# Optimization experiments

Measured on AMD Instinct MI355X. Metric: run time of the kernel, lower is better.

Reference implementation:

```python
import jax, jax.numpy as jnp
import numpy as np

B, N, T, F_IN = 4, 2000, 24, 16
H = 128          # hidden_dim
E = 64000        # num edges
C = 6            # num_classes (LOS A-F)
NH = 1           # num_horizons


def setup_inputs() -> dict:
    key = jax.random.key(0)
    ks = jax.random.split(key, 16)
    s = lambda *sh: 1.0 / np.sqrt(sh[-1])
    inp = {
        "node_features": jax.random.normal(ks[0], (B, N, T, F_IN), dtype=jnp.float32),
        "edge_index": jax.random.randint(ks[1], (2, E), 0, N, dtype=jnp.int64),
        # GRU (single layer, unidirectional), PyTorch gate order r,z,n
        "W_ih": jax.random.normal(ks[2], (3 * H, F_IN), dtype=jnp.float32) * s(3 * H, F_IN),
        "W_hh": jax.random.normal(ks[3], (3 * H, H), dtype=jnp.float32) * s(3 * H, H),
        "b_ih": jnp.zeros((3 * H,), dtype=jnp.float32),
        "b_hh": jnp.zeros((3 * H,), dtype=jnp.float32),
        # two GCN layers (H -> H)
        "gcn_W1": jax.random.normal(ks[4], (H, H), dtype=jnp.float32) * s(H, H),
        "gcn_b1": jnp.zeros((H,), dtype=jnp.float32),
        "gcn_W2": jax.random.normal(ks[5], (H, H), dtype=jnp.float32) * s(H, H),
        "gcn_b2": jnp.zeros((H,), dtype=jnp.float32),
        # LayerNorms
        "ln_g1": jnp.ones((H,), dtype=jnp.float32),
        "ln_b1": jnp.zeros((H,), dtype=jnp.float32),
        "ln_g2": jnp.ones((H,), dtype=jnp.float32),
        "ln_b2": jnp.zeros((H,), dtype=jnp.float32),
        # classifier: Linear(2H -> H), ReLU, Linear(H -> C*NH)
        "cls_W1": jax.random.normal(ks[6], (H, 2 * H), dtype=jnp.float32) * s(H, 2 * H),
        "cls_b1": jnp.zeros((H,), dtype=jnp.float32),
        "cls_W2": jax.random.normal(ks[7], (C * NH, H), dtype=jnp.float32) * s(C * NH, H),
        "cls_b2": jnp.zeros((C * NH,), dtype=jnp.float32),
    }
    return inp


def _gru(x, W_ih, W_hh, b_ih, b_hh):
    # x: [BN, T, F] -> final hidden [BN, H]
    BN = x.shape[0]
    gi = jnp.einsum('btf,gf->btg', x, W_ih) + b_ih           # [BN, T, 3H]
    h0 = jnp.zeros((BN, H), dtype=x.dtype)

    def step(h, gi_t):
        gh = h @ W_hh.T + b_hh
        ir, iz, inn = jnp.split(gi_t, 3, axis=-1)
        hr, hz, hn = jnp.split(gh, 3, axis=-1)
        r = jax.nn.sigmoid(ir + hr)
        z = jax.nn.sigmoid(iz + hz)
        n = jnp.tanh(inn + r * hn)
        h_new = (1.0 - z) * n + z * h
        return h_new, None

    h_fin, _ = jax.lax.scan(step, h0, jnp.swapaxes(gi, 0, 1))  # scan over time
    return h_fin


def _gcn(x, src, dst, W, b):
    # x: [B, N, D]; normalized adjacency aggregation then linear
    deg = jax.ops.segment_sum(jnp.ones((src.shape[0],), x.dtype), dst, num_segments=N)
    deg = jnp.maximum(deg, 1.0)
    dis = deg ** -0.5
    norm = dis[src] * dis[dst]                                # [E]
    msg = x[:, src, :] * norm[None, :, None]                  # [B, E, D]
    agg = jax.vmap(lambda m: jax.ops.segment_sum(m, dst, num_segments=N))(msg)
    return agg @ W.T + b


def _layernorm(x, g, b, eps=1e-5):
    mu = jnp.mean(x, axis=-1, keepdims=True)
    var = jnp.var(x, axis=-1, keepdims=True)
    return (x - mu) * jax.lax.rsqrt(var + eps) * g + b


def reference(node_features, edge_index, W_ih, W_hh, b_ih, b_hh,
              gcn_W1, gcn_b1, gcn_W2, gcn_b2,
              ln_g1, ln_b1, ln_g2, ln_b2,
              cls_W1, cls_b1, cls_W2, cls_b2):
    src, dst = edge_index[0], edge_index[1]
    x = node_features.reshape(B * N, T, F_IN)
    temporal = _gru(x, W_ih, W_hh, b_ih, b_hh).reshape(B, N, H)   # [B, N, H]

    s = _gcn(temporal, src, dst, gcn_W1, gcn_b1)
    s = jax.nn.relu(_layernorm(s, ln_g1, ln_b1))
    s = _gcn(s, src, dst, gcn_W2, gcn_b2)
    s = jax.nn.relu(_layernorm(s, ln_g2, ln_b2))

    combined = jnp.concatenate([temporal, s], axis=-1)            # [B, N, 2H]
    h = jax.nn.relu(combined @ cls_W1.T + cls_b1)
    logits = h @ cls_W2.T + cls_b2
    return logits.reshape(B, N, NH, C)
```

## Files before the change

kernel.cpp:

```cpp
#include <hip/hip_runtime.h>
#include <math.h>

#define BB  4
#define NN  2000
#define TT  24
#define FIN 16
#define HH  128
#define EE  64000
#define CC  6
#define BN  (BB*NN)
#define SLOTC 128

typedef _Float16 f16x8 __attribute__((ext_vector_type(8)));
typedef float f32x4 __attribute__((ext_vector_type(4)));

#define HP2 136
#define GRUB 500

__global__ __launch_bounds__(512) void gru_fill_kernel(
    const float* __restrict__ x,
    const float* __restrict__ W_hh,
    const float* __restrict__ W_ih,
    const float* __restrict__ b_ih, const float* __restrict__ b_hh,
    const float* __restrict__ gW1,
    const float* __restrict__ cW1,
    _Float16* __restrict__ tw16,
    _Float16* __restrict__ tc16,
    const int* __restrict__ src, const int* __restrict__ dst,
    int* __restrict__ cnt, int* __restrict__ slots)
{
    const int tid  = threadIdx.x;

    if (blockIdx.x >= GRUB) {
        int e = (blockIdx.x - GRUB) * 512 + tid;
        if (e < EE) {
            int d = dst[e], s = src[e];
            int pos = atomicAdd(&cnt[d], 1);
            if (pos < SLOTC) slots[d * SLOTC + pos] = s;
        }
        return;
    }

    const int lane = tid & 63;
    const int w    = tid >> 6;
    const int l15  = lane & 15;
    const int lg   = lane >> 4;
    const int m0   = blockIdx.x * 16;
    const int u    = w * 16 + l15;

    __shared__ __align__(16) unsigned short Hhi[2][16][HP2];
    __shared__ __align__(16) unsigned short Xhi[TT][16][FIN];

    f16x8 Bh[3][4];
    #pragma unroll
    for (int g = 0; g < 3; ++g) {
        const int col = g * 128 + u;
        #pragma unroll
        for (int kf = 0; kf < 4; ++kf) {
            const float* wp = W_hh + col * 128 + kf * 32 + lg * 8;
            float4 c0 = *(const float4*)wp;
            float4 c1 = *(const float4*)(wp + 4);
            f16x8 b;
            b[0] = (_Float16)c0.x; b[1] = (_Float16)c0.y;
            b[2] = (_Float16)c0.z; b[3] = (_Float16)c0.w;
            b[4] = (_Float16)c1.x; b[5] = (_Float16)c1.y;
            b[6] = (_Float16)c1.z; b[7] = (_Float16)c1.w;
            Bh[g][kf] = b;
        }
    }
    f16x8 Bi[3];
    #pragma unroll
    for (int g = 0; g < 3; ++g) {
        const int col = g * 128 + u;
        f16x8 b;
        #pragma unroll
        for (int i = 0; i < 8; ++i) b[i] = (_Float16)0.0f;
        if (lg < 2) {
            const float* wp = W_ih + col * 16 + lg * 8;
            float4 c0 = *(const float4*)wp;
            float4 c1 = *(const float4*)(wp + 4);
            b[0] = (_Float16)c0.x; b[1] = (_Float16)c0.y;
            b[2] = (_Float16)c0.z; b[3] = (_Float16)c0.w;
            b[4] = (_Float16)c1.x; b[5] = (_Float16)c1.y;
            b[6] = (_Float16)c1.z; b[7] = (_Float16)c1.w;
        } else if (lg == 2) {
            float bias = b_ih[col] + ((g < 2) ? b_hh[col] : 0.0f);
            b[0] = (_Float16)bias;
        }
        Bi[g] = b;
    }

    const float bhn = b_hh[256 + u];
    float hprev[4] = {0.0f, 0.0f, 0.0f, 0.0f};

    for (int i = tid; i < TT * 16 * FIN; i += 512) {
        int t   = i >> 8;
        int rem = i & 255;
        int seq = rem >> 4;
        int f   = rem & 15;
        float v = x[(size_t)(m0 + seq) * (TT * FIN) + t * FIN + f];
        _Float16 hb = (_Float16)v;
        Xhi[t][seq][f] = *(unsigned short*)&hb;
    }
    for (int i = tid; i < 16 * HP2; i += 512) (&Hhi[0][0][0])[i] = 0;
    __syncthreads();

    const f32x4 Z4 = (f32x4){0.f, 0.f, 0.f, 0.f};
    f32x4 aR, aZ, aH, aI;

#define IH_SHADOW(tt) do { \
        f16x8 axh; \
        _Float16 zz = (_Float16)0.0f; \
        axh = (f16x8){zz,zz,zz,zz,zz,zz,zz,zz}; \
        if (lg < 2) { \
            axh = *(const f16x8*)&Xhi[tt][l15][lg * 8]; \
        } else if (lg == 2) { \
            axh[0] = (_Float16)1.0f; \
        } \
        aR = __builtin_amdgcn_mfma_f32_16x16x32_f16(axh, Bi[0], Z4, 0, 0, 0); \
        aZ = __builtin_amdgcn_mfma_f32_16x16x32_f16(axh, Bi[1], Z4, 0, 0, 0); \
        aI = __builtin_amdgcn_mfma_f32_16x16x32_f16(axh, Bi[2], Z4, 0, 0, 0); \
        aH = Z4; \
    } while (0)

    IH_SHADOW(0);

    for (int t = 0; t < TT; ++t) {
        const int rb = t & 1, wb = rb ^ 1;

        #pragma unroll
        for (int kf = 0; kf < 4; ++kf) {
            const int ko = kf * 32 + lg * 8;
            f16x8 ahh = *(const f16x8*)&Hhi[rb][l15][ko];
            aR = __builtin_amdgcn_mfma_f32_16x16x32_f16(ahh, Bh[0][kf], aR, 0, 0, 0);
            aZ = __builtin_amdgcn_mfma_f32_16x16x32_f16(ahh, Bh[1][kf], aZ, 0, 0, 0);
            aH = __builtin_amdgcn_mfma_f32_16x16x32_f16(ahh, Bh[2][kf], aH, 0, 0, 0);
        }

        f32x4 aRv = aR, aZv = aZ, aHv = aH, aIv = aI;

        #pragma unroll
        for (int p = 0; p < 4; ++p) {
            float r = __builtin_amdgcn_rcpf(1.0f + __expf(-aRv[p]));
            float z = __builtin_amdgcn_rcpf(1.0f + __expf(-aZv[p]));
            float pre = fmaf(r, aHv[p] + bhn, aIv[p]);
            float e2 = __expf(2.0f * pre);
            float n = fmaf(-2.0f, __builtin_amdgcn_rcpf(e2 + 1.0f), 1.0f);
            float h = fmaf(z, hprev[p] - n, n);
            hprev[p] = h;
            _Float16 hb = (_Float16)h;
            const int seq = lg * 4 + p;
            Hhi[wb][seq][u] = *(unsigned short*)&hb;
        }

        if (t + 1 < TT) IH_SHADOW(t + 1);
        __syncthreads();
    }
#undef IH_SHADOW

    {
        f32x4 accw = Z4, accc = Z4;
        #pragma unroll
        for (int kf = 0; kf < 4; ++kf) {
            const int ko = kf * 32 + lg * 8;
            f16x8 ah = *(const f16x8*)&Hhi[0][l15][ko];

            const float* wp = gW1 + (size_t)u * 128 + ko;
            float4 c0 = *(const float4*)wp;
            float4 c1 = *(const float4*)(wp + 4);
            f16x8 bw;
            bw[0] = (_Float16)c0.x; bw[1] = (_Float16)c0.y;
            bw[2] = (_Float16)c0.z; bw[3] = (_Float16)c0.w;
            bw[4] = (_Float16)c1.x; bw[5] = (_Float16)c1.y;
            bw[6] = (_Float16)c1.z; bw[7] = (_Float16)c1.w;
            accw = __builtin_amdgcn_mfma_f32_16x16x32_f16(ah, bw, accw, 0, 0, 0);

            const float* cp = cW1 + (size_t)u * 256 + ko;
            float4 d0 = *(const float4*)cp;
            float4 d1 = *(const float4*)(cp + 4);
            f16x8 bc;
            bc[0] = (_Float16)d0.x; bc[1] = (_Float16)d0.y;
            bc[2] = (_Float16)d0.z; bc[3] = (_Float16)d0.w;
            bc[4] = (_Float16)d1.x; bc[5] = (_Float16)d1.y;
            bc[6] = (_Float16)d1.z; bc[7] = (_Float16)d1.w;
            accc = __builtin_amdgcn_mfma_f32_16x16x32_f16(ah, bc, accc, 0, 0, 0);
        }
        #pragma unroll
        for (int p = 0; p < 4; ++p) {
            const int row = lg * 4 + p;
            tw16[(size_t)(m0 + row) * HH + u] = (_Float16)accw[p];
            tc16[(size_t)(m0 + row) * HH + u] = (_Float16)accc[p];
        }
    }
}

__global__ __launch_bounds__(1024) void gcn1b_kernel(
    const _Float16* __restrict__ tw,
    const int* __restrict__ cnt, const int* __restrict__ slots,
    const float* __restrict__ gb1,
    const float* __restrict__ lg1, const float* __restrict__ lb1,
    const float* __restrict__ gW2,
    _Float16* __restrict__ sw)
{
    const int tid  = threadIdx.x;
    const int nd   = tid >> 8;
    const int t8   = tid & 255;
    const int j    = t8 & 127;
    const int half = t8 >> 7;
    const int n0   = blockIdx.x * 4;
    const int n    = n0 + nd;

    __shared__ float disL[2048];
    for (int i = tid; i < 2048; i += 1024)
        disL[i] = rsqrtf(fmaxf((float)cnt[i], 1.0f));
    __syncthreads();

    const int deg = min(cnt[n], SLOTC);
    const float rd = disL[n];
    const int mid = (deg + 1) >> 1;
    int e        = half ? mid : 0;
    const int e1 = half ? deg : mid;
    const int* sl = slots + (size_t)n * SLOTC;

    float a0 = 0.f, a1 = 0.f, a2 = 0.f, a3 = 0.f;
    for (; e + 1 < e1; e += 2) {
        int   s0 = sl[e],      s1i = sl[e + 1];
        float m0 = disL[s0],   m1  = disL[s1i];
        const _Float16* p0 = tw + (size_t)s0  * HH + j;
        const _Float16* p1 = tw + (size_t)s1i * HH + j;
        a0 = fmaf(m0, (float)p0[0],       a0); a1 = fmaf(m0, (float)p0[NN*HH],   a1);
        a2 = fmaf(m0, (float)p0[2*NN*HH], a2); a3 = fmaf(m0, (float)p0[3*NN*HH], a3);
        a0 = fmaf(m1, (float)p1[0],       a0); a1 = fmaf(m1, (float)p1[NN*HH],   a1);
        a2 = fmaf(m1, (float)p1[2*NN*HH], a2); a3 = fmaf(m1, (float)p1[3*NN*HH], a3);
    }
    if (e < e1) {
        int s0 = sl[e]; float m0 = disL[s0];
        const _Float16* p0 = tw + (size_t)s0 * HH + j;
        a0 = fmaf(m0, (float)p0[0],       a0); a1 = fmaf(m0, (float)p0[NN*HH],   a1);
        a2 = fmaf(m0, (float)p0[2*NN*HH], a2); a3 = fmaf(m0, (float)p0[3*NN*HH], a3);
    }

    __shared__ __align__(16) float pagg[4][BB][HH];
    __shared__ __align__(16) float agg[4][BB][HH];
    if (half) {
        pagg[nd][0][j] = a0; pagg[nd][1][j] = a1;
        pagg[nd][2][j] = a2; pagg[nd][3][j] = a3;
    }
    __syncthreads();
    if (!half) {
        agg[nd][0][j] = a0 + pagg[nd][0][j]; agg[nd][1][j] = a1 + pagg[nd][1][j];
        agg[nd][2][j] = a2 + pagg[nd][2][j]; agg[nd][3][j] = a3 + pagg[nd][3][j];
    }
    __syncthreads();

    const float bj = gb1[j];
    const int b0 = half * 2, b1 = half * 2 + 1;
    float c0 = fmaf(rd, agg[nd][b0][j], bj);
    float c1 = fmaf(rd, agg[nd][b1][j], bj);

    const int lane = t8 & 63, wv = (t8 >> 6) & 1;
    __shared__ float red[4][2][2][2][2];
    {
        float s1 = c0, s2 = c0 * c0;
        for (int off = 32; off >= 1; off >>= 1) { s1 += __shfl_down(s1, off); s2 += __shfl_down(s2, off); }
        if (lane == 0) { red[nd][half][wv][0][0] = s1; red[nd][half][wv][0][1] = s2; }
        s1 = c1; s2 = c1 * c1;
        for (int off = 32; off >= 1; off >>= 1) { s1 += __shfl_down(s1, off); s2 += __shfl_down(s2, off); }
        if (lane == 0) { red[nd][half][wv][1][0] = s1; red[nd][half][wv][1][1] = s2; }
    }
    __syncthreads();

    __shared__ __align__(16) unsigned short sL[16][HP2];
    const float gj = lg1[j], btj = lb1[j];
    #pragma unroll
    for (int q = 0; q < 2; ++q) {
        float cv = q ? c1 : c0;
        float s1 = red[nd][half][0][q][0] + red[nd][half][1][q][0];
        float s2 = red[nd][half][0][q][1] + red[nd][half][1][q][1];
        float mu = s1 * (1.0f / HH);
        float var = s2 * (1.0f / HH) - mu * mu;
        float y = (cv - mu) * rsqrtf(var + 1e-5f) * gj + btj;
        _Float16 hv = (_Float16)fmaxf(y, 0.0f);
        sL[nd * 4 + (half * 2 + q)][j] = *(unsigned short*)&hv;
    }
    __syncthreads();

    if (tid < 512) {
        const int w = tid >> 6, l15 = tid & 15, lg = (tid & 63) >> 4;
        const int u = w * 16 + l15;
        f32x4 acc = (f32x4){0.f, 0.f, 0.f, 0.f};
        #pragma unroll
        for (int kf = 0; kf < 4; ++kf) {
            const int ko = kf * 32 + lg * 8;
            f16x8 a = *(const f16x8*)&sL[l15][ko];
            const float* wp = gW2 + (size_t)u * 128 + ko;
            float4 c0v = *(const float4*)wp;
            float4 c1v = *(const float4*)(wp + 4);
            f16x8 b;
            b[0] = (_Float16)c0v.x; b[1] = (_Float16)c0v.y;
            b[2] = (_Float16)c0v.z; b[3] = (_Float16)c0v.w;
            b[4] = (_Float16)c1v.x; b[5] = (_Float16)c1v.y;
            b[6] = (_Float16)c1v.z; b[7] = (_Float16)c1v.w;
            acc = __builtin_amdgcn_mfma_f32_16x16x32_f16(a, b, acc, 0, 0, 0);
        }
        #pragma unroll
        for (int p = 0; p < 4; ++p) {
            const int r = lg * 4 + p;
            const int nd2 = r >> 2, b2 = r & 3;
            sw[((size_t)b2 * NN + n0 + nd2) * HH + u] = (_Float16)acc[p];
        }
    }
}

__global__ __launch_bounds__(1024) void gcn2b_cls_kernel(
    const _Float16* __restrict__ sw,
    const int* __restrict__ cnt, const int* __restrict__ slots,
    const float* __restrict__ gb2,
    const float* __restrict__ lg2, const float* __restrict__ lb2,
    const float* __restrict__ cW1,
    const _Float16* __restrict__ tc,
    const float* __restrict__ cb1,
    const float* __restrict__ cW2,
    const float* __restrict__ cb2,
    float* __restrict__ out)
{
    const int tid  = threadIdx.x;
    const int nd   = tid >> 8;
    const int t8   = tid & 255;
    const int j    = t8 & 127;
    const int half = t8 >> 7;
    const int n0   = blockIdx.x * 4;
    const int n    = n0 + nd;

    __shared__ float disL[2048];
    for (int i = tid; i < 2048; i += 1024)
        disL[i] = rsqrtf(fmaxf((float)cnt[i], 1.0f));
    __syncthreads();

    const int deg = min(cnt[n], SLOTC);
    const float rd = disL[n];
    const int mid = (deg + 1) >> 1;
    int e        = half ? mid : 0;
    const int e1 = half ? deg : mid;
    const int* sl = slots + (size_t)n * SLOTC;

    float a0 = 0.f, a1 = 0.f, a2 = 0.f, a3 = 0.f;
    for (; e + 1 < e1; e += 2) {
        int   s0 = sl[e],      s1i = sl[e + 1];
        float m0 = disL[s0],   m1  = disL[s1i];
        const _Float16* p0 = sw + (size_t)s0  * HH + j;
        const _Float16* p1 = sw + (size_t)s1i * HH + j;
        a0 = fmaf(m0, (float)p0[0],       a0); a1 = fmaf(m0, (float)p0[NN*HH],   a1);
        a2 = fmaf(m0, (float)p0[2*NN*HH], a2); a3 = fmaf(m0, (float)p0[3*NN*HH], a3);
        a0 = fmaf(m1, (float)p1[0],       a0); a1 = fmaf(m1, (float)p1[NN*HH],   a1);
        a2 = fmaf(m1, (float)p1[2*NN*HH], a2); a3 = fmaf(m1, (float)p1[3*NN*HH], a3);
    }
    if (e < e1) {
        int s0 = sl[e]; float m0 = disL[s0];
        const _Float16* p0 = sw + (size_t)s0 * HH + j;
        a0 = fmaf(m0, (float)p0[0],       a0); a1 = fmaf(m0, (float)p0[NN*HH],   a1);
        a2 = fmaf(m0, (float)p0[2*NN*HH], a2); a3 = fmaf(m0, (float)p0[3*NN*HH], a3);
    }

    __shared__ __align__(16) float pagg[4][BB][HH];
    __shared__ __align__(16) float agg[4][BB][HH];
    if (half) {
        pagg[nd][0][j] = a0; pagg[nd][1][j] = a1;
        pagg[nd][2][j] = a2; pagg[nd][3][j] = a3;
    }
    __syncthreads();
    if (!half) {
        agg[nd][0][j] = a0 + pagg[nd][0][j]; agg[nd][1][j] = a1 + pagg[nd][1][j];
        agg[nd][2][j] = a2 + pagg[nd][2][j]; agg[nd][3][j] = a3 + pagg[nd][3][j];
    }
    __syncthreads();

    const float bj = gb2[j];
    const int b0 = half * 2, b1 = half * 2 + 1;
    float c0 = fmaf(rd, agg[nd][b0][j], bj);
    float c1 = fmaf(rd, agg[nd][b1][j], bj);

    const int lane = t8 & 63, wv = (t8 >> 6) & 1;
    __shared__ float red[4][2][2][2][2];
    {
        float s1 = c0, s2 = c0 * c0;
        for (int off = 32; off >= 1; off >>= 1) { s1 += __shfl_down(s1, off); s2 += __shfl_down(s2, off); }
        if (lane == 0) { red[nd][half][wv][0][0] = s1; red[nd][half][wv][0][1] = s2; }
        s1 = c1; s2 = c1 * c1;
        for (int off = 32; off >= 1; off >>= 1) { s1 += __shfl_down(s1, off); s2 += __shfl_down(s2, off); }
        if (lane == 0) { red[nd][half][wv][1][0] = s1; red[nd][half][wv][1][1] = s2; }
    }
    __syncthreads();

    __shared__ __align__(16) unsigned short s2L[16][HP2];
    const float gj = lg2[j], btj = lb2[j];
    #pragma unroll
    for (int q = 0; q < 2; ++q) {
        float cv = q ? c1 : c0;
        float s1 = red[nd][half][0][q][0] + red[nd][half][1][q][0];
        float s2 = red[nd][half][0][q][1] + red[nd][half][1][q][1];
        float mu = s1 * (1.0f / HH);
        float var = s2 * (1.0f / HH) - mu * mu;
        float y = (cv - mu) * rsqrtf(var + 1e-5f) * gj + btj;
        _Float16 hv = (_Float16)fmaxf(y, 0.0f);
        s2L[nd * 4 + (half * 2 + q)][j] = *(unsigned short*)&hv;
    }
    __syncthreads();

    __shared__ __align__(16) float h1L[16][132];
    if (tid < 512) {
        const int w = tid >> 6, l15 = tid & 15, lg = (tid & 63) >> 4;
        const int u = w * 16 + l15;
        f32x4 acc = (f32x4){0.f, 0.f, 0.f, 0.f};
        #pragma unroll
        for (int kf = 0; kf < 4; ++kf) {
            const int ko = kf * 32 + lg * 8;
            f16x8 a = *(const f16x8*)&s2L[l15][ko];
            const float* cp = cW1 + (size_t)u * 256 + 128 + ko;
            float4 d0 = *(const float4*)cp;
            float4 d1 = *(const float4*)(cp + 4);
            f16x8 b;
            b[0] = (_Float16)d0.x; b[1] = (_Float16)d0.y;
            b[2] = (_Float16)d0.z; b[3] = (_Float16)d0.w;
            b[4] = (_Float16)d1.x; b[5] = (_Float16)d1.y;
            b[6] = (_Float16)d1.z; b[7] = (_Float16)d1.w;
            acc = __builtin_amdgcn_mfma_f32_16x16x32_f16(a, b, acc, 0, 0, 0);
        }
        const float bu = cb1[u];
        #pragma unroll
        for (int p = 0; p < 4; ++p) {
            const int r = lg * 4 + p;
            const int nd2 = r >> 2, b2 = r & 3;
            const size_t flat = (size_t)b2 * NN + n0 + nd2;
            float tcv = (float)tc[flat * HH + u];
            h1L[r][u] = fmaxf(acc[p] + tcv + bu, 0.0f);
        }
    }
    __syncthreads();

    if (tid < 16 * CC) {
        int r = tid / CC, cc = tid - r * CC;
        const int nd2 = r >> 2, b2 = r & 3;
        const size_t flat = (size_t)b2 * NN + n0 + nd2;
        float a = cb2[cc];
        const float* wp = cW2 + cc * HH;
        #pragma unroll 4
        for (int k = 0; k < HH; ++k) a = fmaf(wp[k], h1L[r][k], a);
        out[flat * CC + cc] = a;
    }
}

extern "C" void kernel_launch(void* const* d_in, const int* in_sizes, int n_in,
                              void* d_out, int out_size, void* d_ws, size_t ws_size,
                              hipStream_t stream) {
    const float* x    = (const float*)d_in[0];
    const int*   ei   = (const int*)  d_in[1];
    const float* W_ih = (const float*)d_in[2];
    const float* W_hh = (const float*)d_in[3];
    const float* b_ih = (const float*)d_in[4];
    const float* b_hh = (const float*)d_in[5];
    const float* gW1  = (const float*)d_in[6];
    const float* gb1  = (const float*)d_in[7];
    const float* gW2  = (const float*)d_in[8];
    const float* gb2  = (const float*)d_in[9];
    const float* lg1  = (const float*)d_in[10];
    const float* lb1  = (const float*)d_in[11];
    const float* lg2  = (const float*)d_in[12];
    const float* lb2  = (const float*)d_in[13];
    const float* cW1  = (const float*)d_in[14];
    const float* cb1  = (const float*)d_in[15];
    const float* cW2  = (const float*)d_in[16];
    const float* cb2  = (const float*)d_in[17];
    float* out = (float*)d_out;

    float* ws = (float*)d_ws;
    _Float16* tw16 = (_Float16*)ws;  ws += (size_t)BN * HH / 2;
    _Float16* tc16 = (_Float16*)ws;  ws += (size_t)BN * HH / 2;
    _Float16* sw16 = (_Float16*)ws;  ws += (size_t)BN * HH / 2;
    int* ip      = (int*)ws;
    int* cnt     = ip;  ip += 2048;
    int* slots   = ip;  ip += (size_t)NN * SLOTC;

    const int* srcp = ei;
    const int* dstp = ei + EE;

    hipMemsetAsync(cnt, 0, 2048 * sizeof(int), stream);

    gru_fill_kernel<<<GRUB + EE / 512, 512, 0, stream>>>(
        x, W_hh, W_ih, b_ih, b_hh, gW1, cW1, tw16, tc16,
        srcp, dstp, cnt, slots);

    gcn1b_kernel<<<NN / 4, 1024, 0, stream>>>(tw16, cnt, slots,
                                              gb1, lg1, lb1, gW2, sw16);

    gcn2b_cls_kernel<<<NN / 4, 1024, 0, stream>>>(sw16, cnt, slots,
                                                  gb2, lg2, lb2, cW1, tc16,
                                                  cb1, cW2, cb2, out);
}
```

Measured before the change: 94.13 us.

## Fuse two GCN kernels into one cooperative kernel with grid sync

Merges the first GCN layer kernel and the second GCN+classifier kernel into a single cooperative launch of 250 blocks, each handling 8 nodes in two passes, separated by a grid-wide barrier. The aim is to remove one kernel launch boundary and the repeated disL setup. In exchange each block does twice the serial work with fewer blocks (250 on 256 CUs), adds a grid.sync, and relies on a cooperative launch fitting all 1024-thread blocks co-resident.

Result: slower. 146.5 us (+55.6%).

```diff
diff --git a/kernel.cpp b/kernel.cpp
--- a/kernel.cpp
+++ b/kernel.cpp
@@ -1,5 +1,8 @@
 #include <hip/hip_runtime.h>
+#include <hip/hip_cooperative_groups.h>
 #include <math.h>
+
+namespace cg = cooperative_groups;
 
 #define BB  4
 #define NN  2000
@@ -13,6 +16,11 @@
 
 typedef _Float16 f16x8 __attribute__((ext_vector_type(8)));
 typedef float f32x4 __attribute__((ext_vector_type(4)));
+
+__device__ __forceinline__ unsigned short f2h(float v) {
+    _Float16 h = (_Float16)v;
+    return *(unsigned short*)&h;
+}
 
 #define HP2 136
 #define GRUB 500
@@ -99,8 +107,7 @@
         int seq = rem >> 4;
         int f   = rem & 15;
         float v = x[(size_t)(m0 + seq) * (TT * FIN) + t * FIN + f];
-        _Float16 hb = (_Float16)v;
-        Xhi[t][seq][f] = *(unsigned short*)&hb;
+        Xhi[t][seq][f] = f2h(v);
     }
     for (int i = tid; i < 16 * HP2; i += 512) (&Hhi[0][0][0])[i] = 0;
     __syncthreads();
@@ -148,9 +155,8 @@
             float n = fmaf(-2.0f, __builtin_amdgcn_rcpf(e2 + 1.0f), 1.0f);
             float h = fmaf(z, hprev[p] - n, n);
             hprev[p] = h;
-            _Float16 hb = (_Float16)h;
             const int seq = lg * 4 + p;
-            Hhi[wb][seq][u] = *(unsigned short*)&hb;
+            Hhi[wb][seq][u] = f2h(h);
         }
 
         if (t + 1 < TT) IH_SHADOW(t + 1);
@@ -194,127 +200,13 @@
     }
 }
 
-__global__ __launch_bounds__(1024) void gcn1b_kernel(
+__global__ __launch_bounds__(1024) void gcn_fused_kernel(
     const _Float16* __restrict__ tw,
     const int* __restrict__ cnt, const int* __restrict__ slots,
     const float* __restrict__ gb1,
     const float* __restrict__ lg1, const float* __restrict__ lb1,
     const float* __restrict__ gW2,
-    _Float16* __restrict__ sw)
-{
-    const int tid  = threadIdx.x;
-    const int nd   = tid >> 8;
-    const int t8   = tid & 255;
-    const int j    = t8 & 127;
-    const int half = t8 >> 7;
-    const int n0   = blockIdx.x * 4;
-    const int n    = n0 + nd;
-
-    __shared__ float disL[2048];
-    for (int i = tid; i < 2048; i += 1024)
-        disL[i] = rsqrtf(fmaxf((float)cnt[i], 1.0f));
-    __syncthreads();
-
-    const int deg = min(cnt[n], SLOTC);
-    const float rd = disL[n];
-    const int mid = (deg + 1) >> 1;
-    int e        = half ? mid : 0;
-    const int e1 = half ? deg : mid;
-    const int* sl = slots + (size_t)n * SLOTC;
-
-    float a0 = 0.f, a1 = 0.f, a2 = 0.f, a3 = 0.f;
-    for (; e + 1 < e1; e += 2) {
-        int   s0 = sl[e],      s1i = sl[e + 1];
-        float m0 = disL[s0],   m1  = disL[s1i];
-        const _Float16* p0 = tw + (size_t)s0  * HH + j;
-        const _Float16* p1 = tw + (size_t)s1i * HH + j;
-        a0 = fmaf(m0, (float)p0[0],       a0); a1 = fmaf(m0, (float)p0[NN*HH],   a1);
-        a2 = fmaf(m0, (float)p0[2*NN*HH], a2); a3 = fmaf(m0, (float)p0[3*NN*HH], a3);
-        a0 = fmaf(m1, (float)p1[0],       a0); a1 = fmaf(m1, (float)p1[NN*HH],   a1);
-        a2 = fmaf(m1, (float)p1[2*NN*HH], a2); a3 = fmaf(m1, (float)p1[3*NN*HH], a3);
-    }
-    if (e < e1) {
-        int s0 = sl[e]; float m0 = disL[s0];
-        const _Float16* p0 = tw + (size_t)s0 * HH + j;
-        a0 = fmaf(m0, (float)p0[0],       a0); a1 = fmaf(m0, (float)p0[NN*HH],   a1);
-        a2 = fmaf(m0, (float)p0[2*NN*HH], a2); a3 = fmaf(m0, (float)p0[3*NN*HH], a3);
-    }
-
-    __shared__ __align__(16) float pagg[4][BB][HH];
-    __shared__ __align__(16) float agg[4][BB][HH];
-    if (half) {
-        pagg[nd][0][j] = a0; pagg[nd][1][j] = a1;
-        pagg[nd][2][j] = a2; pagg[nd][3][j] = a3;
-    }
-    __syncthreads();
-    if (!half) {
-        agg[nd][0][j] = a0 + pagg[nd][0][j]; agg[nd][1][j] = a1 + pagg[nd][1][j];
-        agg[nd][2][j] = a2 + pagg[nd][2][j]; agg[nd][3][j] = a3 + pagg[nd][3][j];
-    }
-    __syncthreads();
-
-    const float bj = gb1[j];
-    const int b0 = half * 2, b1 = half * 2 + 1;
-    float c0 = fmaf(rd, agg[nd][b0][j], bj);
-    float c1 = fmaf(rd, agg[nd][b1][j], bj);
-
-    const int lane = t8 & 63, wv = (t8 >> 6) & 1;
-    __shared__ float red[4][2][2][2][2];
-    {
-        float s1 = c0, s2 = c0 * c0;
-        for (int off = 32; off >= 1; off >>= 1) { s1 += __shfl_down(s1, off); s2 += __shfl_down(s2, off); }
-        if (lane == 0) { red[nd][half][wv][0][0] = s1; red[nd][half][wv][0][1] = s2; }
-        s1 = c1; s2 = c1 * c1;
-        for (int off = 32; off >= 1; off >>= 1) { s1 += __shfl_down(s1, off); s2 += __shfl_down(s2, off); }
-        if (lane == 0) { red[nd][half][wv][1][0] = s1; red[nd][half][wv][1][1] = s2; }
-    }
-    __syncthreads();
-
-    __shared__ __align__(16) unsigned short sL[16][HP2];
-    const float gj = lg1[j], btj = lb1[j];
-    #pragma unroll
-    for (int q = 0; q < 2; ++q) {
-        float cv = q ? c1 : c0;
-        float s1 = red[nd][half][0][q][0] + red[nd][half][1][q][0];
-        float s2 = red[nd][half][0][q][1] + red[nd][half][1][q][1];
-        float mu = s1 * (1.0f / HH);
-        float var = s2 * (1.0f / HH) - mu * mu;
-        float y = (cv - mu) * rsqrtf(var + 1e-5f) * gj + btj;
-        _Float16 hv = (_Float16)fmaxf(y, 0.0f);
-        sL[nd * 4 + (half * 2 + q)][j] = *(unsigned short*)&hv;
-    }
-    __syncthreads();
-
-    if (tid < 512) {
-        const int w = tid >> 6, l15 = tid & 15, lg = (tid & 63) >> 4;
-        const int u = w * 16 + l15;
-        f32x4 acc = (f32x4){0.f, 0.f, 0.f, 0.f};
-        #pragma unroll
-        for (int kf = 0; kf < 4; ++kf) {
-            const int ko = kf * 32 + lg * 8;
-            f16x8 a = *(const f16x8*)&sL[l15][ko];
-            const float* wp = gW2 + (size_t)u * 128 + ko;
-            float4 c0v = *(const float4*)wp;
-            float4 c1v = *(const float4*)(wp + 4);
-            f16x8 b;
-            b[0] = (_Float16)c0v.x; b[1] = (_Float16)c0v.y;
-            b[2] = (_Float16)c0v.z; b[3] = (_Float16)c0v.w;
-            b[4] = (_Float16)c1v.x; b[5] = (_Float16)c1v.y;
-            b[6] = (_Float16)c1v.z; b[7] = (_Float16)c1v.w;
-            acc = __builtin_amdgcn_mfma_f32_16x16x32_f16(a, b, acc, 0, 0, 0);
-        }
-        #pragma unroll
-        for (int p = 0; p < 4; ++p) {
-            const int r = lg * 4 + p;
-            const int nd2 = r >> 2, b2 = r & 3;
-            sw[((size_t)b2 * NN + n0 + nd2) * HH + u] = (_Float16)acc[p];
-        }
-    }
-}
-
-__global__ __launch_bounds__(1024) void gcn2b_cls_kernel(
-    const _Float16* __restrict__ sw,
-    const int* __restrict__ cnt, const int* __restrict__ slots,
+    _Float16* __restrict__ sw,
     const float* __restrict__ gb2,
     const float* __restrict__ lg2, const float* __restrict__ lb2,
     const float* __restrict__ cW1,
@@ -324,129 +216,233 @@
     const float* __restrict__ cb2,
     float* __restrict__ out)
 {
+    cg::grid_group grid = cg::this_grid();
+
     const int tid  = threadIdx.x;
     const int nd   = tid >> 8;
     const int t8   = tid & 255;
     const int j    = t8 & 127;
     const int half = t8 >> 7;
-    const int n0   = blockIdx.x * 4;
-    const int n    = n0 + nd;
+    const int n0   = blockIdx.x * 8;
 
     __shared__ float disL[2048];
+    __shared__ __align__(16) float pagg[4][BB][HH];
+    __shared__ __align__(16) float agg[4][BB][HH];
+    __shared__ float red[4][2][2][2][2];
+    __shared__ __align__(16) unsigned short sL[16][HP2];
+    __shared__ __align__(16) float h1L[16][132];
+
     for (int i = tid; i < 2048; i += 1024)
         disL[i] = rsqrtf(fmaxf((float)cnt[i], 1.0f));
     __syncthreads();
 
-    const int deg = min(cnt[n], SLOTC);
-    const float rd = disL[n];
-    const int mid = (deg + 1) >> 1;
-    int e        = half ? mid : 0;
-    const int e1 = half ? deg : mid;
-    const int* sl = slots + (size_t)n * SLOTC;
-
-    float a0 = 0.f, a1 = 0.f, a2 = 0.f, a3 = 0.f;
-    for (; e + 1 < e1; e += 2) {
-        int   s0 = sl[e],      s1i = sl[e + 1];
-        float m0 = disL[s0],   m1  = disL[s1i];
-        const _Float16* p0 = sw + (size_t)s0  * HH + j;
-        const _Float16* p1 = sw + (size_t)s1i * HH + j;
-        a0 = fmaf(m0, (float)p0[0],       a0); a1 = fmaf(m0, (float)p0[NN*HH],   a1);
-        a2 = fmaf(m0, (float)p0[2*NN*HH], a2); a3 = fmaf(m0, (float)p0[3*NN*HH], a3);
-        a0 = fmaf(m1, (float)p1[0],       a0); a1 = fmaf(m1, (float)p1[NN*HH],   a1);
-        a2 = fmaf(m1, (float)p1[2*NN*HH], a2); a3 = fmaf(m1, (float)p1[3*NN*HH], a3);
-    }
-    if (e < e1) {
-        int s0 = sl[e]; float m0 = disL[s0];
-        const _Float16* p0 = sw + (size_t)s0 * HH + j;
-        a0 = fmaf(m0, (float)p0[0],       a0); a1 = fmaf(m0, (float)p0[NN*HH],   a1);
-        a2 = fmaf(m0, (float)p0[2*NN*HH], a2); a3 = fmaf(m0, (float)p0[3*NN*HH], a3);
-    }
-
-    __shared__ __align__(16) float pagg[4][BB][HH];
-    __shared__ __align__(16) float agg[4][BB][HH];
-    if (half) {
-        pagg[nd][0][j] = a0; pagg[nd][1][j] = a1;
-        pagg[nd][2][j] = a2; pagg[nd][3][j] = a3;
-    }
-    __syncthreads();
-    if (!half) {
-        agg[nd][0][j] = a0 + pagg[nd][0][j]; agg[nd][1][j] = a1 + pagg[nd][1][j];
-        agg[nd][2][j] = a2 + pagg[nd][2][j]; agg[nd][3][j] = a3 + pagg[nd][3][j];
-    }
-    __syncthreads();
-
-    const float bj = gb2[j];
-    const int b0 = half * 2, b1 = half * 2 + 1;
-    float c0 = fmaf(rd, agg[nd][b0][j], bj);
-    float c1 = fmaf(rd, agg[nd][b1][j], bj);
-
-    const int lane = t8 & 63, wv = (t8 >> 6) & 1;
-    __shared__ float red[4][2][2][2][2];
-    {
-        float s1 = c0, s2 = c0 * c0;
-        for (int off = 32; off >= 1; off >>= 1) { s1 += __shfl_down(s1, off); s2 += __shfl_down(s2, off); }
-        if (lane == 0) { red[nd][half][wv][0][0] = s1; red[nd][half][wv][0][1] = s2; }
-        s1 = c1; s2 = c1 * c1;
-        for (int off = 32; off >= 1; off >>= 1) { s1 += __shfl_down(s1, off); s2 += __shfl_down(s2, off); }
-        if (lane == 0) { red[nd][half][wv][1][0] = s1; red[nd][half][wv][1][1] = s2; }
-    }
-    __syncthreads();
-
-    __shared__ __align__(16) unsigned short s2L[16][HP2];
-    const float gj = lg2[j], btj = lb2[j];
     #pragma unroll
-    for (int q = 0; q < 2; ++q) {
-        float cv = q ? c1 : c0;
-        float s1 = red[nd][half][0][q][0] + red[nd][half][1][q][0];
-        float s2 = red[nd][half][0][q][1] + red[nd][half][1][q][1];
-        float mu = s1 * (1.0f / HH);
-        float var = s2 * (1.0f / HH) - mu * mu;
-        float y = (cv - mu) * rsqrtf(var + 1e-5f) * gj + btj;
-        _Float16 hv = (_Float16)fmaxf(y, 0.0f);
-        s2L[nd * 4 + (half * 2 + q)][j] = *(unsigned short*)&hv;
-    }
-    __syncthreads();
-
-    __shared__ __align__(16) float h1L[16][132];
-    if (tid < 512) {
-        const int w = tid >> 6, l15 = tid & 15, lg = (tid & 63) >> 4;
-        const int u = w * 16 + l15;
-        f32x4 acc = (f32x4){0.f, 0.f, 0.f, 0.f};
-        #pragma unroll
-        for (int kf = 0; kf < 4; ++kf) {
-            const int ko = kf * 32 + lg * 8;
-            f16x8 a = *(const f16x8*)&s2L[l15][ko];
-            const float* cp = cW1 + (size_t)u * 256 + 128 + ko;
-            float4 d0 = *(const float4*)cp;
-            float4 d1 = *(const float4*)(cp + 4);
-            f16x8 b;
-            b[0] = (_Float16)d0.x; b[1] = (_Float16)d0.y;
-            b[2] = (_Float16)d0.z; b[3] = (_Float16)d0.w;
-            b[4] = (_Float16)d1.x; b[5] = (_Float16)d1.y;
-            b[6] = (_Float16)d1.z; b[7] = (_Float16)d1.w;
-            acc = __builtin_amdgcn_mfma_f32_16x16x32_f16(a, b, acc, 0, 0, 0);
-        }
-        const float bu = cb1[u];
-        #pragma unroll
-        for (int p = 0; p < 4; ++p) {
-            const int r = lg * 4 + p;
+    for (int g = 0; g < 2; ++g) {
+        const int n = n0 + g * 4 + nd;
+        const int deg = min(cnt[n], SLOTC);
+        const float rd = disL[n];
+        const int mid = (deg + 1) >> 1;
+        int e        = half ? mid : 0;
+        const int e1 = half ? deg : mid;
+        const int* sl = slots + (size_t)n * SLOTC;
+
+        float a0 = 0.f, a1 = 0.f, a2 = 0.f, a3 = 0.f;
+        for (; e + 1 < e1; e += 2) {
+            int   s0 = sl[e],      s1i = sl[e + 1];
+            float m0 = disL[s0],   m1  = disL[s1i];
+            const _Float16* p0 = tw + (size_t)s0  * HH + j;
+            const _Float16* p1 = tw + (size_t)s1i * HH + j;
+            a0 = fmaf(m0, (float)p0[0],       a0); a1 = fmaf(m0, (float)p0[NN*HH],   a1);
+            a2 = fmaf(m0, (float)p0[2*NN*HH], a2); a3 = fmaf(m0, (float)p0[3*NN*HH], a3);
+            a0 = fmaf(m1, (float)p1[0],       a0); a1 = fmaf(m1, (float)p1[NN*HH],   a1);
+            a2 = fmaf(m1, (float)p1[2*NN*HH], a2); a3 = fmaf(m1, (float)p1[3*NN*HH], a3);
+        }
+        if (e < e1) {
+            int s0 = sl[e]; float m0 = disL[s0];
+            const _Float16* p0 = tw + (size_t)s0 * HH + j;
+            a0 = fmaf(m0, (float)p0[0],       a0); a1 = fmaf(m0, (float)p0[NN*HH],   a1);
+            a2 = fmaf(m0, (float)p0[2*NN*HH], a2); a3 = fmaf(m0, (float)p0[3*NN*HH], a3);
+        }
+
+        if (half) {
+            pagg[nd][0][j] = a0; pagg[nd][1][j] = a1;
+            pagg[nd][2][j] = a2; pagg[nd][3][j] = a3;
+        }
+        __syncthreads();
+        if (!half) {
+            agg[nd][0][j] = a0 + pagg[nd][0][j]; agg[nd][1][j] = a1 + pagg[nd][1][j];
+            agg[nd][2][j] = a2 + pagg[nd][2][j]; agg[nd][3][j] = a3 + pagg[nd][3][j];
+        }
+        __syncthreads();
+
+        const float bj = gb1[j];
+        const int b0 = half * 2, b1 = half * 2 + 1;
+        float c0 = fmaf(rd, agg[nd][b0][j], bj);
+        float c1 = fmaf(rd, agg[nd][b1][j], bj);
+
+        const int lane = t8 & 63, wv = (t8 >> 6) & 1;
+        {
+            float s1 = c0, s2 = c0 * c0;
+            for (int off = 32; off >= 1; off >>= 1) { s1 += __shfl_down(s1, off); s2 += __shfl_down(s2, off); }
+            if (lane == 0) { red[nd][half][wv][0][0] = s1; red[nd][half][wv][0][1] = s2; }
+            s1 = c1; s2 = c1 * c1;
+            for (int off = 32; off >= 1; off >>= 1) { s1 += __shfl_down(s1, off); s2 += __shfl_down(s2, off); }
+            if (lane == 0) { red[nd][half][wv][1][0] = s1; red[nd][half][wv][1][1] = s2; }
+        }
+        __syncthreads();
+
+        const float gj = lg1[j], btj = lb1[j];
+        #pragma unroll
+        for (int q = 0; q < 2; ++q) {
+            float cv = q ? c1 : c0;
+            float s1 = red[nd][half][0][q][0] + red[nd][half][1][q][0];
+            float s2 = red[nd][half][0][q][1] + red[nd][half][1][q][1];
+            float mu = s1 * (1.0f / HH);
+            float var = s2 * (1.0f / HH) - mu * mu;
+            float y = (cv - mu) * rsqrtf(var + 1e-5f) * gj + btj;
+            sL[nd * 4 + (half * 2 + q)][j] = f2h(fmaxf(y, 0.0f));
+        }
+        __syncthreads();
+
+        if (tid < 512) {
+            const int w = tid >> 6, l15 = tid & 15, lg = (tid & 63) >> 4;
+            const int u = w * 16 + l15;
+            f32x4 acc = (f32x4){0.f, 0.f, 0.f, 0.f};
+            #pragma unroll
+            for (int kf = 0; kf < 4; ++kf) {
+                const int ko = kf * 32 + lg * 8;
+                f16x8 a = *(const f16x8*)&sL[l15][ko];
+                const float* wp = gW2 + (size_t)u * 128 + ko;
+                float4 c0v = *(const float4*)wp;
+                float4 c1v = *(const float4*)(wp + 4);
+                f16x8 b;
+                b[0] = (_Float16)c0v.x; b[1] = (_Float16)c0v.y;
+                b[2] = (_Float16)c0v.z; b[3] = (_Float16)c0v.w;
+                b[4] = (_Float16)c1v.x; b[5] = (_Float16)c1v.y;
+                b[6] = (_Float16)c1v.z; b[7] = (_Float16)c1v.w;
+                acc = __builtin_amdgcn_mfma_f32_16x16x32_f16(a, b, acc, 0, 0, 0);
+            }
+            #pragma unroll
+            for (int p = 0; p < 4; ++p) {
+                const int r = lg * 4 + p;
+                const int nd2 = r >> 2, b2 = r & 3;
+                sw[((size_t)b2 * NN + n0 + g * 4 + nd2) * HH + u] = (_Float16)acc[p];
+            }
+        }
+        __syncthreads();
+    }
+
+    grid.sync();
+
+    #pragma unroll
+    for (int g = 0; g < 2; ++g) {
+        const int n = n0 + g * 4 + nd;
+        const int deg = min(cnt[n], SLOTC);
+        const float rd = disL[n];
+        const int mid = (deg + 1) >> 1;
+        int e        = half ? mid : 0;
+        const int e1 = half ? deg : mid;
+        const int* sl = slots + (size_t)n * SLOTC;
+
+        float a0 = 0.f, a1 = 0.f, a2 = 0.f, a3 = 0.f;
+        for (; e + 1 < e1; e += 2) {
+            int   s0 = sl[e],      s1i = sl[e + 1];
+            float m0 = disL[s0],   m1  = disL[s1i];
+            const _Float16* p0 = sw + (size_t)s0  * HH + j;
+            const _Float16* p1 = sw + (size_t)s1i * HH + j;
+            a0 = fmaf(m0, (float)p0[0],       a0); a1 = fmaf(m0, (float)p0[NN*HH],   a1);
+            a2 = fmaf(m0, (float)p0[2*NN*HH], a2); a3 = fmaf(m0, (float)p0[3*NN*HH], a3);
+            a0 = fmaf(m1, (float)p1[0],       a0); a1 = fmaf(m1, (float)p1[NN*HH],   a1);
+            a2 = fmaf(m1, (float)p1[2*NN*HH], a2); a3 = fmaf(m1, (float)p1[3*NN*HH], a3);
+        }
+        if (e < e1) {
+            int s0 = sl[e]; float m0 = disL[s0];
+            const _Float16* p0 = sw + (size_t)s0 * HH + j;
+            a0 = fmaf(m0, (float)p0[0],       a0); a1 = fmaf(m0, (float)p0[NN*HH],   a1);
+            a2 = fmaf(m0, (float)p0[2*NN*HH], a2); a3 = fmaf(m0, (float)p0[3*NN*HH], a3);
+        }
+
+        if (half) {
+            pagg[nd][0][j] = a0; pagg[nd][1][j] = a1;
+            pagg[nd][2][j] = a2; pagg[nd][3][j] = a3;
+        }
+        __syncthreads();
+        if (!half) {
+            agg[nd][0][j] = a0 + pagg[nd][0][j]; agg[nd][1][j] = a1 + pagg[nd][1][j];
+            agg[nd][2][j] = a2 + pagg[nd][2][j]; agg[nd][3][j] = a3 + pagg[nd][3][j];
+        }
+        __syncthreads();
+
+        const float bj = gb2[j];
+        const int b0 = half * 2, b1 = half * 2 + 1;
+        float c0 = fmaf(rd, agg[nd][b0][j], bj);
+        float c1 = fmaf(rd, agg[nd][b1][j], bj);
+
+        const int lane = t8 & 63, wv = (t8 >> 6) & 1;
+        {
+            float s1 = c0, s2 = c0 * c0;
+            for (int off = 32; off >= 1; off >>= 1) { s1 += __shfl_down(s1, off); s2 += __shfl_down(s2, off); }
+            if (lane == 0) { red[nd][half][wv][0][0] = s1; red[nd][half][wv][0][1] = s2; }
+            s1 = c1; s2 = c1 * c1;
+            for (int off = 32; off >= 1; off >>= 1) { s1 += __shfl_down(s1, off); s2 += __shfl_down(s2, off); }
+            if (lane == 0) { red[nd][half][wv][1][0] = s1; red[nd][half][wv][1][1] = s2; }
+        }
+        __syncthreads();
+
+        const float gj = lg2[j], btj = lb2[j];
+        #pragma unroll
+        for (int q = 0; q < 2; ++q) {
+            float cv = q ? c1 : c0;
+            float s1 = red[nd][half][0][q][0] + red[nd][half][1][q][0];
+            float s2 = red[nd][half][0][q][1] + red[nd][half][1][q][1];
+            float mu = s1 * (1.0f / HH);
+            float var = s2 * (1.0f / HH) - mu * mu;
+            float y = (cv - mu) * rsqrtf(var + 1e-5f) * gj + btj;
+            sL[nd * 4 + (half * 2 + q)][j] = f2h(fmaxf(y, 0.0f));
+        }
+        __syncthreads();
+
+        if (tid < 512) {
+            const int w = tid >> 6, l15 = tid & 15, lg = (tid & 63) >> 4;
+            const int u = w * 16 + l15;
+            f32x4 acc = (f32x4){0.f, 0.f, 0.f, 0.f};
+            #pragma unroll
+            for (int kf = 0; kf < 4; ++kf) {
+                const int ko = kf * 32 + lg * 8;
+                f16x8 a = *(const f16x8*)&sL[l15][ko];
+                const float* cp = cW1 + (size_t)u * 256 + 128 + ko;
+                float4 d0 = *(const float4*)cp;
+                float4 d1 = *(const float4*)(cp + 4);
+                f16x8 b;
+                b[0] = (_Float16)d0.x; b[1] = (_Float16)d0.y;
+                b[2] = (_Float16)d0.z; b[3] = (_Float16)d0.w;
+                b[4] = (_Float16)d1.x; b[5] = (_Float16)d1.y;
+                b[6] = (_Float16)d1.z; b[7] = (_Float16)d1.w;
+                acc = __builtin_amdgcn_mfma_f32_16x16x32_f16(a, b, acc, 0, 0, 0);
+            }
+            const float bu = cb1[u];
+            #pragma unroll
+            for (int p = 0; p < 4; ++p) {
+                const int r = lg * 4 + p;
+                const int nd2 = r >> 2, b2 = r & 3;
+                const size_t flat = (size_t)b2 * NN + n0 + g * 4 + nd2;
+                float tcv = (float)tc[flat * HH + u];
+                h1L[r][u] = fmaxf(acc[p] + tcv + bu, 0.0f);
+            }
+        }
+        __syncthreads();
+
+        if (tid < 16 * CC) {
+            int r = tid / CC, cc = tid - r * CC;
             const int nd2 = r >> 2, b2 = r & 3;
-            const size_t flat = (size_t)b2 * NN + n0 + nd2;
-            float tcv = (float)tc[flat * HH + u];
-            h1L[r][u] = fmaxf(acc[p] + tcv + bu, 0.0f);
-        }
-    }
-    __syncthreads();
-
-    if (tid < 16 * CC) {
-        int r = tid / CC, cc = tid - r * CC;
-        const int nd2 = r >> 2, b2 = r & 3;
-        const size_t flat = (size_t)b2 * NN + n0 + nd2;
-        float a = cb2[cc];
-        const float* wp = cW2 + cc * HH;
-        #pragma unroll 4
-        for (int k = 0; k < HH; ++k) a = fmaf(wp[k], h1L[r][k], a);
-        out[flat * CC + cc] = a;
+            const size_t flat = (size_t)b2 * NN + n0 + g * 4 + nd2;
+            float a = cb2[cc];
+            const float* wp = cW2 + cc * HH;
+            #pragma unroll 4
+            for (int k = 0; k < HH; ++k) a = fmaf(wp[k], h1L[r][k], a);
+            out[flat * CC + cc] = a;
+        }
+        __syncthreads();
     }
 }
 
@@ -490,10 +486,16 @@
         x, W_hh, W_ih, b_ih, b_hh, gW1, cW1, tw16, tc16,
         srcp, dstp, cnt, slots);
 
-    gcn1b_kernel<<<NN / 4, 1024, 0, stream>>>(tw16, cnt, slots,
-                                              gb1, lg1, lb1, gW2, sw16);
-
-    gcn2b_cls_kernel<<<NN / 4, 1024, 0, stream>>>(sw16, cnt, slots,
-                                                  gb2, lg2, lb2, cW1, tc16,
-                                                  cb1, cW2, cb2, out);
+    {
+        void* args[] = {
+            (void*)&tw16, (void*)&cnt, (void*)&slots,
+            (void*)&gb1, (void*)&lg1, (void*)&lb1, (void*)&gW2,
+            (void*)&sw16,
+            (void*)&gb2, (void*)&lg2, (void*)&lb2,
+            (void*)&cW1, (void*)&tc16, (void*)&cb1,
+            (void*)&cW2, (void*)&cb2, (void*)&out
+        };
+        hipLaunchCooperativeKernel((const void*)gcn_fused_kernel,
+                                   dim3(NN / 8), dim3(1024), args, 0, stream);
+    }
 }
```
